# Performance work log

Hardware: AMD Instinct MI355X
Metric: run time of the kernel (lower is better)

## Reference

```python
import jax, jax.numpy as jnp
import numpy as np

DT = 0.01
EPS = 1e-5


def setup_inputs() -> dict:
    key = jax.random.key(0)
    ks = jax.random.split(key, 20)
    B, H, IN, COV, CH, OH, OUT = 1024, 64, 8, 16, 64, 128, 2
    NE, OPE = 400, 256            # events, observations per event
    TOT = NE * OPE

    def w(k, sh, sc=0.05):
        return jax.random.normal(k, sh, dtype=jnp.float32) * sc

    return {
        'time_uniq': jnp.arange(NE, dtype=jnp.float32) * DT,   # event k fires at grid step k
        'time_ptr': jnp.arange(NE + 1, dtype=jnp.int32) * OPE,  # uniform obs per event
        'X': jax.random.normal(ks[0], (TOT, IN), dtype=jnp.float32),
        'sample_ids': jax.random.randint(ks[1], (TOT,), 0, B, dtype=jnp.int32),
        'covs': jax.random.normal(ks[2], (B, COV), dtype=jnp.float32),
        'T': 5,
        'cov_W1': w(ks[3], (CH, COV)), 'cov_b1': jnp.zeros((CH,), jnp.float32),
        'cov_W2': w(ks[4], (H, CH)),   'cov_b2': jnp.zeros((H,), jnp.float32),
        'gb_Wih': w(ks[5], (3 * H, IN)), 'gb_Whh': w(ks[6], (3 * H, H)),
        'gb_bih': jnp.zeros((3 * H,), jnp.float32), 'gb_bhh': jnp.zeros((3 * H,), jnp.float32),
        'gx_W': w(ks[7], (3 * H, 1)), 'gx_b': jnp.zeros((3 * H,), jnp.float32),
        'ghr_W': w(ks[8], (H, H)), 'ghz_W': w(ks[9], (H, H)), 'ghh_W': w(ks[10], (H, H)),
        'out_W1': w(ks[11], (OH, H)), 'out_b1': jnp.zeros((OH,), jnp.float32),
        'out_W2': w(ks[12], (OUT, OH)), 'out_b2': jnp.zeros((OUT,), jnp.float32),
    }


def _forward(time_uniq, time_ptr, X, sample_ids, covs, T,
             cov_W1, cov_b1, cov_W2, cov_b2,
             gb_Wih, gb_Whh, gb_bih, gb_bhh,
             gx_W, gx_b, ghr_W, ghz_W, ghh_W,
             out_W1, out_b1, out_W2, out_b2):
    n_events = time_uniq.shape[0]
    ope = X.shape[0] // n_events          # uniform observations per event (static)
    n_steps = int(round(T / DT))
    delta_t = DT

    # covariates_map (dropout p=0 -> identity)
    h0 = jnp.tanh(jnp.maximum(covs @ cov_W1.T + cov_b1, 0.0) @ cov_W2.T + cov_b2)

    def gru_bayes(x, h):                  # torch.nn.GRUCell semantics (gates r,z,n)
        gi = x @ gb_Wih.T + gb_bih
        gh = h @ gb_Whh.T + gb_bhh
        ir, iz, inn = jnp.split(gi, 3, axis=1)
        hr, hz, hn = jnp.split(gh, 3, axis=1)
        r = jax.nn.sigmoid(ir + hr)
        z = jax.nn.sigmoid(iz + hz)
        n = jnp.tanh(inn + r * hn)
        return (1.0 - z) * n + z * h

    def gru_ode(h):                       # FullGRUODECell with x = zeros
        px = jnp.zeros((h.shape[0], 1), h.dtype)
        gx = px @ gx_W.T + gx_b
        xr, xz, xh = jnp.split(gx, 3, axis=1)
        r = jax.nn.sigmoid(xr + h @ ghr_W.T)
        z = jax.nn.sigmoid(xz + h @ ghz_W.T)
        u = jnp.tanh(xh + (r * h) @ ghh_W.T)
        return h + delta_t * (1.0 - z) * (u - h)

    times = jnp.arange(n_steps, dtype=jnp.float32) * DT
    offs = jnp.arange(ope)

    def step(carry, t):
        h, i = carry
        ic = jnp.minimum(i, n_events - 1)
        fire = (i < n_events) & (time_uniq[ic] <= t + EPS)   # <=1 event per grid step
        obs = time_ptr[ic] + offs
        idx = sample_ids[obs]
        h_upd = h.at[idx].set(gru_bayes(X[obs], h[idx]))
        h = jnp.where(fire, h_upd, h)
        i = i + fire.astype(i.dtype)
        h_rec = h                          # recorded after events, before ODE step
        h = gru_ode(h)
        return (h, i), h_rec

    (h_last, _), h_steps = jax.lax.scan(step, (h0, jnp.int32(0)), times)
    h_path = jnp.concatenate([h_steps, h_last[None]], axis=0)   # [n_steps+1, B, H]

    # net_out (dropout p=0 -> identity)
    o = jnp.maximum(jnp.einsum('tbh,oh->tbo', h_path, out_W1) + out_b1, 0.0)
    return jnp.einsum('tbh,oh->tbo', o, out_W2) + out_b2


def reference(time_uniq, time_ptr, X, sample_ids, covs, T,
              cov_W1, cov_b1, cov_W2, cov_b2,
              gb_Wih, gb_Whh, gb_bih, gb_bhh,
              gx_W, gx_b, ghr_W, ghz_W, ghh_W,
              out_W1, out_b1, out_W2, out_b2):
    return _forward(time_uniq, time_ptr, X, sample_ids, covs, T,
                    cov_W1, cov_b1, cov_W2, cov_b2,
                    gb_Wih, gb_Whh, gb_bih, gb_bhh,
                    gx_W, gx_b, ghr_W, ghz_W, ghh_W,
                    out_W1, out_b1, out_W2, out_b2)
```

## Files before the change

### kernel.cpp

```cpp
#include <hip/hip_runtime.h>

#define DT_F 0.01f
#define EPS_F 1e-5f
#define NEG_INF_I (-1073741824)

typedef _Float16 f16;
typedef _Float16 f16x2 __attribute__((ext_vector_type(2)));
typedef _Float16 f16x8 __attribute__((ext_vector_type(8)));
typedef float f32x4 __attribute__((ext_vector_type(4)));

#define MFMA16(a, b, c) __builtin_amdgcn_mfma_f32_16x16x32_f16((a), (b), (c), 0, 0, 0)

__device__ __forceinline__ float rl(float v, int l) {
  return __int_as_float(__builtin_amdgcn_readlane(__float_as_int(v), l));
}
__device__ __forceinline__ float sigm(float x) {
  float e = __builtin_amdgcn_exp2f(-1.442695041f * x);
  return __builtin_amdgcn_rcpf(1.0f + e);
}
__device__ __forceinline__ float tanhf_fast(float x) {
  float e = __builtin_amdgcn_exp2f(2.885390082f * x);
  return fmaf(-2.0f, __builtin_amdgcn_rcpf(e + 1.0f), 1.0f);
}
__device__ __forceinline__ float dot2(unsigned w, unsigned h, float acc) {
  return __builtin_amdgcn_fdot2(__builtin_bit_cast(f16x2, w),
                                __builtin_bit_cast(f16x2, h), acc, false);
}
__device__ __forceinline__ unsigned packf16(float a, float b) {
  return __builtin_bit_cast(unsigned, __builtin_amdgcn_cvt_pkrtz(a, b));
}
#define ANCH4(v) asm volatile("" : "+v"((v).x), "+v"((v).y), "+v"((v).z), "+v"((v).w))
#define ANCHF(v) asm volatile("" : "+v"(v))

__global__ void build_evtab_kernel(const int* __restrict__ sample_ids,
                                   const int* __restrict__ time_ptr,
                                   int* __restrict__ evtab, int B, int ope) {
  int k = blockIdx.x;
  int base = time_ptr[k];
  for (int t = threadIdx.x; t < ope; t += blockDim.x) {
    int obs = base + t;
    int sid = sample_ids[obs];
    atomicMax(&evtab[k * B + sid], obs + 1);
  }
}

__global__ void pack_pairs_kernel(const float* __restrict__ ghr,
                                  const float* __restrict__ ghz,
                                  const float* __restrict__ ghh,
                                  const float* __restrict__ gbWhh,
                                  const float* __restrict__ gbWih,
                                  unsigned* __restrict__ odeP,
                                  unsigned* __restrict__ bayP,
                                  unsigned* __restrict__ wihP, int IN) {
  int idx = blockIdx.x * 256 + threadIdx.x;
  if (idx < 3 * 64 * 32) {
    int p = idx & 31, r = idx >> 5;
    int g = r >> 6, i = r & 63;
    const float* src = (g == 0) ? ghr : ((g == 1) ? ghz : ghh);
    odeP[idx] = packf16(src[i * 64 + 2 * p], src[i * 64 + 2 * p + 1]);
    bayP[idx] = packf16(gbWhh[r * 64 + 2 * p], gbWhh[r * 64 + 2 * p + 1]);
  }
  if (idx < 3 * 64 * 4) {
    int p = idx & 3, r = idx >> 2;
    float a = (2 * p < IN) ? gbWih[r * IN + 2 * p] : 0.0f;
    float b = (2 * p + 1 < IN) ? gbWih[r * IN + 2 * p + 1] : 0.0f;
    wihP[idx] = packf16(a, b);
  }
}

__global__ void pack_head_kernel(const float* __restrict__ W1, f16* __restrict__ w1P) {
  int f = blockIdx.x;
  int l = threadIdx.x;
  int t = f >> 1, kf = f & 1;
  int n = 16 * t + (l & 15);
  for (int j = 0; j < 8; ++j) {
    int k = 8 * (l >> 4) + j + 32 * kf;
    w1P[f * 512 + l * 8 + j] = (f16)W1[n * 64 + k];
  }
}

__global__ __launch_bounds__(256, 1) void evolve_kernel(
    const float* __restrict__ time_uniq,
    const float* __restrict__ X,
    const float* __restrict__ covs,
    const float* __restrict__ cov_W1, const float* __restrict__ cov_b1,
    const float* __restrict__ cov_W2, const float* __restrict__ cov_b2,
    const float* __restrict__ gb_bih, const float* __restrict__ gb_bhh,
    const float* __restrict__ gx_b,
    const unsigned* __restrict__ odeP, const unsigned* __restrict__ bayP,
    const unsigned* __restrict__ wihP,
    const int* __restrict__ evtab,
    f16* __restrict__ hp16,
    int B, int NE, int n_steps, int IN, int COV)
{
  __shared__ unsigned sBW[3 * 64 * 32];
  __shared__ int sStep[1024];
  __shared__ __align__(16) f16 sH16[4][64];
  __shared__ __align__(16) f16 sRH16[4][64];

  const int tid = threadIdx.x;
  const int wid = tid >> 6, lane = tid & 63;
  const int b = blockIdx.x * 4 + wid;
  const bool alive = (b < B);

  for (int idx = tid; idx < 3 * 64 * 32; idx += 256) {
    int c = idx & 31, r = idx >> 5;
    int i = r & 63, s = c >> 2;
    sBW[r * 32 + (((s ^ (i & 7)) << 2) | (c & 3))] = bayP[idx];
  }
  if (wid == 0) {
    int pm = NEG_INF_I;
    int loc[16];
#pragma unroll
    for (int j = 0; j < 16; ++j) {
      int e = lane * 16 + j;
      int gv = NEG_INF_I;
      if (e < NE && e < 1024) {
        float tu = time_uniq[e];
        int k0 = (int)floorf((tu - EPS_F) * 100.0f) - 2;
        if (k0 < 0) k0 = 0;
        while ((float)k0 * DT_F + EPS_F < tu) ++k0;
        gv = k0 - e;
      }
      pm = max(pm, gv);
      loc[j] = pm;
    }
    int tot = pm;
#pragma unroll
    for (int off = 1; off < 64; off <<= 1) {
      int v = __shfl_up(tot, off);
      if (lane >= off) tot = max(tot, v);
    }
    int excl = __shfl_up(tot, 1);
    if (lane == 0) excl = NEG_INF_I;
#pragma unroll
    for (int j = 0; j < 16; ++j)
      sStep[lane * 16 + j] = lane * 16 + j + max(loc[j], excl);
  }
  __syncthreads();

  const uint4* odeQ = (const uint4*)odeP;
  uint4 WR[8], WZ[8], WU[8];
#pragma unroll
  for (int q = 0; q < 8; ++q) {
    WR[q] = odeQ[(0 * 64 + lane) * 8 + q];
    WZ[q] = odeQ[(1 * 64 + lane) * 8 + q];
    WU[q] = odeQ[(2 * 64 + lane) * 8 + q];
  }
#pragma unroll
  for (int q = 0; q < 8; ++q) { ANCH4(WR[q]); ANCH4(WZ[q]); ANCH4(WU[q]); }

  const uint4* wihQ = (const uint4*)wihP;

  float xr = gx_b[lane], xz = gx_b[64 + lane], xh = gx_b[128 + lane];
  float crz_r = gb_bih[lane] + gb_bhh[lane];
  float crz_z = gb_bih[64 + lane] + gb_bhh[64 + lane];
  float bihn = gb_bih[128 + lane], bhhn = gb_bhh[128 + lane];
  ANCHF(xr); ANCHF(xz); ANCHF(xh); ANCHF(crz_r); ANCHF(crz_z);
  ANCHF(bihn); ANCHF(bhhn);

  float h = 0.0f;
  if (alive) {
    float cacc = cov_b1[lane];
    for (int c = 0; c < COV; ++c)
      cacc = fmaf(covs[b * COV + c], cov_W1[lane * COV + c], cacc);
    float cl = fmaxf(cacc, 0.0f);
    float hacc = cov_b2[lane];
#pragma unroll
    for (int j = 0; j < 64; ++j)
      hacc = fmaf(rl(cl, j), cov_W2[lane * 64 + j], hacc);
    h = tanhf_fast(hacc);
  }
  sH16[wid][lane] = (f16)h;

  int e_next = 0, s_next = 0x7fffffff, v_cur = 0, v_pipe = 0;
  float xf[8];
#pragma unroll
  for (int kk = 0; kk < 8; ++kk) xf[kk] = 0.0f;
  if (alive && NE > 0) {
    s_next = sStep[0];
    v_cur = evtab[b];
    if (v_cur > 0) {
      const float* xp = X + (long)(v_cur - 1) * IN;
#pragma unroll
      for (int kk = 0; kk < 8; ++kk) xf[kk] = (kk < IN) ? xp[kk] : 0.0f;
    }
    v_pipe = (NE > 1) ? evtab[B + b] : 0;
  } else if (NE > 0) {
    s_next = sStep[0];
  }

  const uint4* hq4 = (const uint4*)sH16[wid];
  const uint4* rq4 = (const uint4*)sRH16[wid];
  f16* hps = hp16 + (long)b * 64 + lane;
  const long rowstride = (long)B * 64;

#pragma unroll 1
  for (int k = 0; k < n_steps; ++k) {
    if (k == s_next) {
      if (v_cur > 0) {
        unsigned xp0 = packf16(xf[0], xf[1]), xp1 = packf16(xf[2], xf[3]);
        unsigned xp2 = packf16(xf[4], xf[5]), xp3 = packf16(xf[6], xf[7]);
        uint4 wxr = wihQ[lane], wxz = wihQ[64 + lane], wxn = wihQ[128 + lane];
        float ar = crz_r, az = crz_z, anh = bhhn, ani = bihn;
        ar = dot2(wxr.x, xp0, ar); ar = dot2(wxr.y, xp1, ar);
        ar = dot2(wxr.z, xp2, ar); ar = dot2(wxr.w, xp3, ar);
        az = dot2(wxz.x, xp0, az); az = dot2(wxz.y, xp1, az);
        az = dot2(wxz.z, xp2, az); az = dot2(wxz.w, xp3, az);
        ani = dot2(wxn.x, xp0, ani); ani = dot2(wxn.y, xp1, ani);
        ani = dot2(wxn.z, xp2, ani); ani = dot2(wxn.w, xp3, ani);
        float ar1 = 0.f, az1 = 0.f, an1 = 0.f;
#pragma unroll
        for (int q = 0; q < 8; ++q) {
          uint4 hh = hq4[q];
          int sw = ((q ^ (lane & 7)) << 2);
          uint4 br = *(const uint4*)&sBW[(0 * 64 + lane) * 32 + sw];
          uint4 bz = *(const uint4*)&sBW[(1 * 64 + lane) * 32 + sw];
          uint4 bn = *(const uint4*)&sBW[(2 * 64 + lane) * 32 + sw];
          ar  = dot2(br.x, hh.x, ar);   ar1 = dot2(br.y, hh.y, ar1);
          ar  = dot2(br.z, hh.z, ar);   ar1 = dot2(br.w, hh.w, ar1);
          az  = dot2(bz.x, hh.x, az);   az1 = dot2(bz.y, hh.y, az1);
          az  = dot2(bz.z, hh.z, az);   az1 = dot2(bz.w, hh.w, az1);
          anh = dot2(bn.x, hh.x, anh);  an1 = dot2(bn.y, hh.y, an1);
          anh = dot2(bn.z, hh.z, anh);  an1 = dot2(bn.w, hh.w, an1);
        }
        float r = sigm(ar + ar1);
        float z = sigm(az + az1);
        float n = tanhf_fast(ani + r * (anh + an1));
        h = (1.0f - z) * n + z * h;
        sH16[wid][lane] = (f16)h;
      }
      ++e_next;
      if (e_next < NE && e_next < 1024) {
        s_next = sStep[e_next];
        v_cur = v_pipe;
        if (v_cur > 0) {
          const float* xp = X + (long)(v_cur - 1) * IN;
#pragma unroll
          for (int kk = 0; kk < 8; ++kk) xf[kk] = (kk < IN) ? xp[kk] : 0.0f;
        }
        v_pipe = (e_next + 1 < NE) ? evtab[(long)(e_next + 1) * B + b] : 0;
      } else {
        s_next = 0x7fffffff;
        v_cur = 0;
      }
    }

    if (alive)
      hps[(long)k * rowstride] = (f16)h;

    float ar0 = xr, ar1 = 0.f, ar2 = 0.f, ar3 = 0.f;
    float az0 = xz, az1 = 0.f, az2 = 0.f, az3 = 0.f;
#pragma unroll
    for (int q = 0; q < 8; ++q) {
      uint4 hp = hq4[q];
      ar0 = dot2(WR[q].x, hp.x, ar0); ar1 = dot2(WR[q].y, hp.y, ar1);
      ar2 = dot2(WR[q].z, hp.z, ar2); ar3 = dot2(WR[q].w, hp.w, ar3);
      az0 = dot2(WZ[q].x, hp.x, az0); az1 = dot2(WZ[q].y, hp.y, az1);
      az2 = dot2(WZ[q].z, hp.z, az2); az3 = dot2(WZ[q].w, hp.w, az3);
    }
    float r = sigm((ar0 + ar1) + (ar2 + ar3));
    float z = sigm((az0 + az1) + (az2 + az3));
    sRH16[wid][lane] = (f16)(r * h);

    float au0 = xh, au1 = 0.f, au2 = 0.f, au3 = 0.f;
#pragma unroll
    for (int q = 0; q < 8; ++q) {
      uint4 rp = rq4[q];
      au0 = dot2(WU[q].x, rp.x, au0); au1 = dot2(WU[q].y, rp.y, au1);
      au2 = dot2(WU[q].z, rp.z, au2); au3 = dot2(WU[q].w, rp.w, au3);
    }
    float u = tanhf_fast((au0 + au1) + (au2 + au3));
    h = fmaf(DT_F * (1.0f - z), u - h, h);
    sH16[wid][lane] = (f16)h;
  }

  if (alive)
    hps[(long)n_steps * rowstride] = (f16)h;
}

__global__ __launch_bounds__(256, 4) void head_mfma_kernel(
    const f16* __restrict__ hp16, const f16* __restrict__ w1P,
    const float* __restrict__ b1, const float* __restrict__ W2,
    const float* __restrict__ b2, float* __restrict__ out, long nrows)
{
  const int wq = threadIdx.x >> 6, lane = threadIdx.x & 63;
  const int col = lane & 15;
  const long rowbase = ((long)blockIdx.x * 4 + wq) * 64;

  f16x8 Wf[8][2];
#pragma unroll
  for (int t = 0; t < 8; ++t)
#pragma unroll
    for (int kf = 0; kf < 2; ++kf)
      Wf[t][kf] = ((const f16x8*)w1P)[(2 * t + kf) * 64 + lane];

  float b1v[8], w2a[8], w2b[8];
#pragma unroll
  for (int t = 0; t < 8; ++t) {
    b1v[t] = b1[16 * t + col];
    w2a[t] = W2[16 * t + col];
    w2b[t] = W2[128 + 16 * t + col];
  }
  const float b20 = b2[0], b21 = b2[1];

#pragma unroll 1
  for (int g = 0; g < 4; ++g) {
    long row0 = rowbase + g * 16;
    long arow = row0 + col;
    f16x8 aH0 = {0, 0, 0, 0, 0, 0, 0, 0}, aH1 = aH0;
    if (arow < nrows) {
      const f16x8* ap = (const f16x8*)(hp16 + arow * 64);
      aH0 = ap[lane >> 4];
      aH1 = ap[(lane >> 4) + 4];
    }
    float p0[4] = {0.f, 0.f, 0.f, 0.f}, p1[4] = {0.f, 0.f, 0.f, 0.f};
#pragma unroll
    for (int t = 0; t < 8; ++t) {
      f32x4 c = {0.f, 0.f, 0.f, 0.f};
      c = MFMA16(aH0, Wf[t][0], c);
      c = MFMA16(aH1, Wf[t][1], c);
#pragma unroll
      for (int i = 0; i < 4; ++i) {
        float o = fmaxf(c[i] + b1v[t], 0.0f);
        p0[i] = fmaf(o, w2a[t], p0[i]);
        p1[i] = fmaf(o, w2b[t], p1[i]);
      }
    }
#pragma unroll
    for (int off = 1; off < 16; off <<= 1) {
#pragma unroll
      for (int i = 0; i < 4; ++i) {
        p0[i] += __shfl_xor(p0[i], off);
        p1[i] += __shfl_xor(p1[i], off);
      }
    }
    if (col == 0) {
#pragma unroll
      for (int i = 0; i < 4; ++i) {
        long row = row0 + (lane >> 4) * 4 + i;
        if (row < nrows) {
          out[row * 2 + 0] = p0[i] + b20;
          out[row * 2 + 1] = p1[i] + b21;
        }
      }
    }
  }
}

extern "C" void kernel_launch(void* const* d_in, const int* in_sizes, int n_in,
                              void* d_out, int out_size, void* d_ws, size_t ws_size,
                              hipStream_t stream) {
  const float* time_uniq  = (const float*)d_in[0];
  const int*   time_ptr   = (const int*)d_in[1];
  const float* X          = (const float*)d_in[2];
  const int*   sample_ids = (const int*)d_in[3];
  const float* covs       = (const float*)d_in[4];
  const float* cov_W1     = (const float*)d_in[6];
  const float* cov_b1     = (const float*)d_in[7];
  const float* cov_W2     = (const float*)d_in[8];
  const float* cov_b2     = (const float*)d_in[9];
  const float* gb_Wih     = (const float*)d_in[10];
  const float* gb_Whh     = (const float*)d_in[11];
  const float* gb_bih     = (const float*)d_in[12];
  const float* gb_bhh     = (const float*)d_in[13];
  const float* gx_b       = (const float*)d_in[15];
  const float* ghr_W      = (const float*)d_in[16];
  const float* ghz_W      = (const float*)d_in[17];
  const float* ghh_W      = (const float*)d_in[18];
  const float* out_W1     = (const float*)d_in[19];
  const float* out_b1     = (const float*)d_in[20];
  const float* out_W2     = (const float*)d_in[21];
  const float* out_b2     = (const float*)d_in[22];

  int NE   = in_sizes[0];
  int TOT  = in_sizes[3];
  int IN   = in_sizes[2] / TOT;
  int CH   = in_sizes[7];
  int COV  = in_sizes[6] / CH;
  int B    = in_sizes[4] / COV;
  int OUTD = in_sizes[22];
  int n_steps = out_size / (B * OUTD) - 1;
  int OPE  = TOT / NE;

  char* ws = (char*)d_ws;
  int* evtab = (int*)ws;
  size_t evbytes = (size_t)NE * (size_t)B * sizeof(int);
  size_t off1 = (evbytes + 255) & ~(size_t)255;
  unsigned* odeP = (unsigned*)(ws + off1);
  unsigned* bayP = odeP + 3 * 64 * 32;
  unsigned* wihP = bayP + 3 * 64 * 32;
  size_t off2 = off1 + (((3 * 64 * 32 * 2 + 3 * 64 * 4) * sizeof(unsigned) + 255) & ~(size_t)255);
  f16* w1P = (f16*)(ws + off2);
  size_t off3 = off2 + ((16 * 512 * sizeof(f16) + 255) & ~(size_t)255);
  f16* hp16 = (f16*)(ws + off3);

  hipMemsetAsync(evtab, 0, evbytes, stream);
  build_evtab_kernel<<<NE, 256, 0, stream>>>(sample_ids, time_ptr, evtab, B, OPE);
  pack_pairs_kernel<<<24, 256, 0, stream>>>(ghr_W, ghz_W, ghh_W, gb_Whh, gb_Wih,
                                            odeP, bayP, wihP, IN);
  pack_head_kernel<<<16, 64, 0, stream>>>(out_W1, w1P);
  evolve_kernel<<<(B + 3) / 4, 256, 0, stream>>>(
      time_uniq, X, covs, cov_W1, cov_b1, cov_W2, cov_b2,
      gb_bih, gb_bhh, gx_b, odeP, bayP, wihP,
      evtab, hp16, B, NE, n_steps, IN, COV);
  long nrows = (long)(n_steps + 1) * B;
  int hb = (int)((nrows + 255) / 256);
  head_mfma_kernel<<<hb, 256, 0, stream>>>(hp16, w1P, out_b1, out_W2, out_b2,
                                           (float*)d_out, nrows);
}
```

Before: 447.3 us.

## Broadcast hidden state via readlane into registers and transpose event table

Replaces the per-wave LDS staging of h and r*h with a cross-lane broadcast: neighbouring lanes are packed into f16 pairs and 32 readlanes place the whole vector in scalar/uniform registers for the dot products. This removes LDS writes and reads and their latency from the sequential 500-step recurrence. The event table is also transposed to sample-major with a fixed 1024-event stride, so each wave reads its own row contiguously. The memset grows to B*1024 entries, and the readlane chain adds scalar instructions and register pressure.

```diff
diff --git a/kernel.cpp b/kernel.cpp
--- a/kernel.cpp
+++ b/kernel.cpp
@@ -3,6 +3,7 @@
 #define DT_F 0.01f
 #define EPS_F 1e-5f
 #define NEG_INF_I (-1073741824)
+#define NEC 1024
 
 typedef _Float16 f16;
 typedef _Float16 f16x2 __attribute__((ext_vector_type(2)));
@@ -30,17 +31,27 @@
   return __builtin_bit_cast(unsigned, __builtin_amdgcn_cvt_pkrtz(a, b));
 }
 #define ANCH4(v) asm volatile("" : "+v"((v).x), "+v"((v).y), "+v"((v).z), "+v"((v).w))
-#define ANCHF(v) asm volatile("" : "+v"(v))
+
+#define BCAST(dst, val)                                                    \
+  {                                                                        \
+    float _hn = __shfl_xor((val), 1);                                      \
+    float _a = (lane & 1) ? _hn : (val);                                   \
+    float _b = (lane & 1) ? (val) : _hn;                                   \
+    unsigned _pr = packf16(_a, _b);                                        \
+    _Pragma("unroll")                                                      \
+    for (int _p = 0; _p < 32; ++_p)                                        \
+      (dst)[_p] = (unsigned)__builtin_amdgcn_readlane((int)_pr, 2 * _p);   \
+  }
 
 __global__ void build_evtab_kernel(const int* __restrict__ sample_ids,
                                    const int* __restrict__ time_ptr,
-                                   int* __restrict__ evtab, int B, int ope) {
+                                   int* __restrict__ evtabT, int B, int ope) {
   int k = blockIdx.x;
   int base = time_ptr[k];
   for (int t = threadIdx.x; t < ope; t += blockDim.x) {
     int obs = base + t;
     int sid = sample_ids[obs];
-    atomicMax(&evtab[k * B + sid], obs + 1);
+    atomicMax(&evtabT[(long)sid * NEC + k], obs + 1);
   }
 }
 
@@ -89,19 +100,18 @@
     const float* __restrict__ gx_b,
     const unsigned* __restrict__ odeP, const unsigned* __restrict__ bayP,
     const unsigned* __restrict__ wihP,
-    const int* __restrict__ evtab,
+    const int* __restrict__ evtabT,
     f16* __restrict__ hp16,
     int B, int NE, int n_steps, int IN, int COV)
 {
   __shared__ unsigned sBW[3 * 64 * 32];
   __shared__ int sStep[1024];
-  __shared__ __align__(16) f16 sH16[4][64];
-  __shared__ __align__(16) f16 sRH16[4][64];
 
   const int tid = threadIdx.x;
   const int wid = tid >> 6, lane = tid & 63;
   const int b = blockIdx.x * 4 + wid;
   const bool alive = (b < B);
+  const int necap = (NE < NEC) ? NE : NEC;
 
   for (int idx = tid; idx < 3 * 64 * 32; idx += 256) {
     int c = idx & 31, r = idx >> 5;
@@ -115,7 +125,7 @@
     for (int j = 0; j < 16; ++j) {
       int e = lane * 16 + j;
       int gv = NEG_INF_I;
-      if (e < NE && e < 1024) {
+      if (e < necap) {
         float tu = time_uniq[e];
         int k0 = (int)floorf((tu - EPS_F) * 100.0f) - 2;
         if (k0 < 0) k0 = 0;
@@ -149,15 +159,12 @@
   }
 #pragma unroll
   for (int q = 0; q < 8; ++q) { ANCH4(WR[q]); ANCH4(WZ[q]); ANCH4(WU[q]); }
-
   const uint4* wihQ = (const uint4*)wihP;
 
-  float xr = gx_b[lane], xz = gx_b[64 + lane], xh = gx_b[128 + lane];
-  float crz_r = gb_bih[lane] + gb_bhh[lane];
-  float crz_z = gb_bih[64 + lane] + gb_bhh[64 + lane];
-  float bihn = gb_bih[128 + lane], bhhn = gb_bhh[128 + lane];
-  ANCHF(xr); ANCHF(xz); ANCHF(xh); ANCHF(crz_r); ANCHF(crz_z);
-  ANCHF(bihn); ANCHF(bhhn);
+  const float xr = gx_b[lane], xz = gx_b[64 + lane], xh = gx_b[128 + lane];
+  const float crz_r = gb_bih[lane] + gb_bhh[lane];
+  const float crz_z = gb_bih[64 + lane] + gb_bhh[64 + lane];
+  const float bihn = gb_bih[128 + lane], bhhn = gb_bhh[128 + lane];
 
   float h = 0.0f;
   if (alive) {
@@ -171,27 +178,28 @@
       hacc = fmaf(rl(cl, j), cov_W2[lane * 64 + j], hacc);
     h = tanhf_fast(hacc);
   }
-  sH16[wid][lane] = (f16)h;
-
+
+  unsigned hp[32];
+  BCAST(hp, h);
+
+  const int* evrow = evtabT + (long)b * NEC;
   int e_next = 0, s_next = 0x7fffffff, v_cur = 0, v_pipe = 0;
   float xf[8];
 #pragma unroll
   for (int kk = 0; kk < 8; ++kk) xf[kk] = 0.0f;
-  if (alive && NE > 0) {
+  if (necap > 0) {
     s_next = sStep[0];
-    v_cur = evtab[b];
-    if (v_cur > 0) {
-      const float* xp = X + (long)(v_cur - 1) * IN;
-#pragma unroll
-      for (int kk = 0; kk < 8; ++kk) xf[kk] = (kk < IN) ? xp[kk] : 0.0f;
-    }
-    v_pipe = (NE > 1) ? evtab[B + b] : 0;
-  } else if (NE > 0) {
-    s_next = sStep[0];
-  }
-
-  const uint4* hq4 = (const uint4*)sH16[wid];
-  const uint4* rq4 = (const uint4*)sRH16[wid];
+    if (alive) {
+      v_cur = evrow[0];
+      if (v_cur > 0) {
+        const float* xp = X + (long)(v_cur - 1) * IN;
+#pragma unroll
+        for (int kk = 0; kk < 8; ++kk) xf[kk] = (kk < IN) ? xp[kk] : 0.0f;
+      }
+      v_pipe = (necap > 1) ? evrow[1] : 0;
+    }
+  }
+
   f16* hps = hp16 + (long)b * 64 + lane;
   const long rowstride = (long)B * 64;
 
@@ -212,26 +220,25 @@
         float ar1 = 0.f, az1 = 0.f, an1 = 0.f;
 #pragma unroll
         for (int q = 0; q < 8; ++q) {
-          uint4 hh = hq4[q];
           int sw = ((q ^ (lane & 7)) << 2);
           uint4 br = *(const uint4*)&sBW[(0 * 64 + lane) * 32 + sw];
           uint4 bz = *(const uint4*)&sBW[(1 * 64 + lane) * 32 + sw];
           uint4 bn = *(const uint4*)&sBW[(2 * 64 + lane) * 32 + sw];
-          ar  = dot2(br.x, hh.x, ar);   ar1 = dot2(br.y, hh.y, ar1);
-          ar  = dot2(br.z, hh.z, ar);   ar1 = dot2(br.w, hh.w, ar1);
-          az  = dot2(bz.x, hh.x, az);   az1 = dot2(bz.y, hh.y, az1);
-          az  = dot2(bz.z, hh.z, az);   az1 = dot2(bz.w, hh.w, az1);
-          anh = dot2(bn.x, hh.x, anh);  an1 = dot2(bn.y, hh.y, an1);
-          anh = dot2(bn.z, hh.z, anh);  an1 = dot2(bn.w, hh.w, an1);
+          ar  = dot2(br.x, hp[4 * q + 0], ar);   ar1 = dot2(br.y, hp[4 * q + 1], ar1);
+          ar  = dot2(br.z, hp[4 * q + 2], ar);   ar1 = dot2(br.w, hp[4 * q + 3], ar1);
+          az  = dot2(bz.x, hp[4 * q + 0], az);   az1 = dot2(bz.y, hp[4 * q + 1], az1);
+          az  = dot2(bz.z, hp[4 * q + 2], az);   az1 = dot2(bz.w, hp[4 * q + 3], az1);
+          anh = dot2(bn.x, hp[4 * q + 0], anh);  an1 = dot2(bn.y, hp[4 * q + 1], an1);
+          anh = dot2(bn.z, hp[4 * q + 2], anh);  an1 = dot2(bn.w, hp[4 * q + 3], an1);
         }
         float r = sigm(ar + ar1);
         float z = sigm(az + az1);
         float n = tanhf_fast(ani + r * (anh + an1));
         h = (1.0f - z) * n + z * h;
-        sH16[wid][lane] = (f16)h;
+        BCAST(hp, h);
       }
       ++e_next;
-      if (e_next < NE && e_next < 1024) {
+      if (e_next < necap) {
         s_next = sStep[e_next];
         v_cur = v_pipe;
         if (v_cur > 0) {
@@ -239,7 +246,7 @@
 #pragma unroll
           for (int kk = 0; kk < 8; ++kk) xf[kk] = (kk < IN) ? xp[kk] : 0.0f;
         }
-        v_pipe = (e_next + 1 < NE) ? evtab[(long)(e_next + 1) * B + b] : 0;
+        v_pipe = (alive && e_next + 1 < necap) ? evrow[e_next + 1] : 0;
       } else {
         s_next = 0x7fffffff;
         v_cur = 0;
@@ -247,36 +254,37 @@
     }
 
     if (alive)
-      hps[(long)k * rowstride] = (f16)h;
+      *hps = (f16)h;
+    hps += rowstride;
 
     float ar0 = xr, ar1 = 0.f, ar2 = 0.f, ar3 = 0.f;
     float az0 = xz, az1 = 0.f, az2 = 0.f, az3 = 0.f;
 #pragma unroll
     for (int q = 0; q < 8; ++q) {
-      uint4 hp = hq4[q];
-      ar0 = dot2(WR[q].x, hp.x, ar0); ar1 = dot2(WR[q].y, hp.y, ar1);
-      ar2 = dot2(WR[q].z, hp.z, ar2); ar3 = dot2(WR[q].w, hp.w, ar3);
-      az0 = dot2(WZ[q].x, hp.x, az0); az1 = dot2(WZ[q].y, hp.y, az1);
-      az2 = dot2(WZ[q].z, hp.z, az2); az3 = dot2(WZ[q].w, hp.w, az3);
+      ar0 = dot2(WR[q].x, hp[4 * q + 0], ar0); ar1 = dot2(WR[q].y, hp[4 * q + 1], ar1);
+      ar2 = dot2(WR[q].z, hp[4 * q + 2], ar2); ar3 = dot2(WR[q].w, hp[4 * q + 3], ar3);
+      az0 = dot2(WZ[q].x, hp[4 * q + 0], az0); az1 = dot2(WZ[q].y, hp[4 * q + 1], az1);
+      az2 = dot2(WZ[q].z, hp[4 * q + 2], az2); az3 = dot2(WZ[q].w, hp[4 * q + 3], az3);
     }
     float r = sigm((ar0 + ar1) + (ar2 + ar3));
     float z = sigm((az0 + az1) + (az2 + az3));
-    sRH16[wid][lane] = (f16)(r * h);
-
+
+    float rh = r * h;
+    unsigned rp[32];
+    BCAST(rp, rh);
     float au0 = xh, au1 = 0.f, au2 = 0.f, au3 = 0.f;
 #pragma unroll
     for (int q = 0; q < 8; ++q) {
-      uint4 rp = rq4[q];
-      au0 = dot2(WU[q].x, rp.x, au0); au1 = dot2(WU[q].y, rp.y, au1);
-      au2 = dot2(WU[q].z, rp.z, au2); au3 = dot2(WU[q].w, rp.w, au3);
+      au0 = dot2(WU[q].x, rp[4 * q + 0], au0); au1 = dot2(WU[q].y, rp[4 * q + 1], au1);
+      au2 = dot2(WU[q].z, rp[4 * q + 2], au2); au3 = dot2(WU[q].w, rp[4 * q + 3], au3);
     }
     float u = tanhf_fast((au0 + au1) + (au2 + au3));
     h = fmaf(DT_F * (1.0f - z), u - h, h);
-    sH16[wid][lane] = (f16)h;
+    BCAST(hp, h);
   }
 
   if (alive)
-    hps[(long)n_steps * rowstride] = (f16)h;
+    *hps = (f16)h;
 }
 
 __global__ __launch_bounds__(256, 4) void head_mfma_kernel(
@@ -384,8 +392,8 @@
   int OPE  = TOT / NE;
 
   char* ws = (char*)d_ws;
-  int* evtab = (int*)ws;
-  size_t evbytes = (size_t)NE * (size_t)B * sizeof(int);
+  int* evtabT = (int*)ws;
+  size_t evbytes = (size_t)B * NEC * sizeof(int);
   size_t off1 = (evbytes + 255) & ~(size_t)255;
   unsigned* odeP = (unsigned*)(ws + off1);
   unsigned* bayP = odeP + 3 * 64 * 32;
@@ -395,15 +403,15 @@
   size_t off3 = off2 + ((16 * 512 * sizeof(f16) + 255) & ~(size_t)255);
   f16* hp16 = (f16*)(ws + off3);
 
-  hipMemsetAsync(evtab, 0, evbytes, stream);
-  build_evtab_kernel<<<NE, 256, 0, stream>>>(sample_ids, time_ptr, evtab, B, OPE);
+  hipMemsetAsync(evtabT, 0, evbytes, stream);
+  build_evtab_kernel<<<NE, 256, 0, stream>>>(sample_ids, time_ptr, evtabT, B, OPE);
   pack_pairs_kernel<<<24, 256, 0, stream>>>(ghr_W, ghz_W, ghh_W, gb_Whh, gb_Wih,
                                             odeP, bayP, wihP, IN);
   pack_head_kernel<<<16, 64, 0, stream>>>(out_W1, w1P);
   evolve_kernel<<<(B + 3) / 4, 256, 0, stream>>>(
       time_uniq, X, covs, cov_W1, cov_b1, cov_W2, cov_b2,
       gb_bih, gb_bhh, gx_b, odeP, bayP, wihP,
-      evtab, hp16, B, NE, n_steps, IN, COV);
+      evtabT, hp16, B, NE, n_steps, IN, COV);
   long nrows = (long)(n_steps + 1) * B;
   int hb = (int)((nrows + 255) / 256);
   head_mfma_kernel<<<hb, 256, 0, stream>>>(hp16, w1P, out_b1, out_W2, out_b2,
```

After: 499.5 us. 1.12x slower.
